# Kernel optimization log

Measured on AMD Instinct MI355X. Metric: run time of the kernel, lower is better.

The kernel has to match this reference:

```python
import jax, jax.numpy as jnp
import numpy as np

N_NODES = 100_000
N_EDGES = 3_200_000
VOCAB = 50_000
D = 256
L_GNN = 4
L_LIN = 2
OUT = 10          # label_size=10 -> output_size=10
N_TGT = 8192
EPS = 1e-5


def layer_norm(x, g, b):
    mu = jnp.mean(x, axis=-1, keepdims=True)
    var = jnp.mean((x - mu) ** 2, axis=-1, keepdims=True)
    return (x - mu) * jax.lax.rsqrt(var + EPS) * g + b


def gcn_conv(x, src, dst, W, b, n):
    # PyG GCNConv defaults: add self loops, symmetric D^-1/2 (A+I) D^-1/2 norm
    h = x @ W                                   # [n, D]
    loops = jnp.arange(n, dtype=src.dtype)
    src2 = jnp.concatenate([src, loops])        # [E+n]
    dst2 = jnp.concatenate([dst, loops])
    deg = jax.ops.segment_sum(jnp.ones(src2.shape[0], dtype=h.dtype), dst2, n)
    dinv = jnp.where(deg > 0, jax.lax.rsqrt(deg), 0.0)
    norm = dinv[src2] * dinv[dst2]              # [E+n]
    out = jax.ops.segment_sum(h[src2] * norm[:, None], dst2, n)  # [n, D]
    return out + b


def setup_inputs() -> dict:
    key = jax.random.key(0)
    ks = jax.random.split(key, 16)
    tokens = jax.random.randint(ks[0], (N_NODES,), 0, VOCAB, dtype=jnp.int32)
    edges = jax.random.randint(ks[1], (2, N_EDGES), 0, N_NODES, dtype=jnp.int32)
    target_indices = jax.random.randint(ks[2], (N_TGT,), 0, N_NODES, dtype=jnp.int32)
    s = 0.05
    emb_table = jax.random.normal(ks[3], (VOCAB, D), jnp.float32)
    gnn_W = jax.random.normal(ks[4], (L_GNN, D, D), jnp.float32) * s
    gnn_b = jnp.zeros((L_GNN, D), jnp.float32)
    gnn_gamma = jnp.ones((L_GNN, D), jnp.float32)
    gnn_beta = jnp.zeros((L_GNN, D), jnp.float32)
    lin_W = jax.random.normal(ks[5], (L_LIN, D, D), jnp.float32) * s
    lin_b = jnp.zeros((L_LIN, D), jnp.float32)
    lin_gamma = jnp.ones((L_LIN, D), jnp.float32)
    lin_beta = jnp.zeros((L_LIN, D), jnp.float32)
    out_W = jax.random.normal(ks[6], (D, OUT), jnp.float32) * s
    out_b = jnp.zeros((OUT,), jnp.float32)
    return {"tokens": tokens, "edges": edges, "target_indices": target_indices,
            "emb_table": emb_table, "gnn_W": gnn_W, "gnn_b": gnn_b,
            "gnn_gamma": gnn_gamma, "gnn_beta": gnn_beta,
            "lin_W": lin_W, "lin_b": lin_b, "lin_gamma": lin_gamma,
            "lin_beta": lin_beta, "out_W": out_W, "out_b": out_b}


def reference(tokens, edges, target_indices, emb_table, gnn_W, gnn_b,
              gnn_gamma, gnn_beta, lin_W, lin_b, lin_gamma, lin_beta,
              out_W, out_b):
    x = emb_table[tokens]                       # [N, D] embedding lookup
    src, dst = edges[0], edges[1]
    for i in range(L_GNN):
        x = gcn_conv(x, src, dst, gnn_W[i], gnn_b[i], N_NODES)
        x = layer_norm(x, gnn_gamma[i], gnn_beta[i])
        x = jax.nn.relu(x)
    x = x[target_indices]                       # [N_TGT, D]
    for i in range(L_LIN):
        x = x @ lin_W[i] + lin_b[i]
        x = layer_norm(x, lin_gamma[i], lin_beta[i])
        x = jax.nn.relu(x)
    return x @ out_W + out_b                    # [N_TGT, OUT]
```

## Files before the change

### kernel.cpp

```cpp
#include <hip/hip_runtime.h>
#include <hip/hip_fp16.h>

#define NN 100000
#define NE 3200000
#define DD 256
#define NT 8192
#define NOUT 10
#define NBUCK 196
#define CSRP_CAP (NE + NBUCK * 4112 + 64)

typedef unsigned short u16;
typedef unsigned int u32;
typedef unsigned char u8;
typedef __attribute__((ext_vector_type(8))) short bf16x8;
typedef __attribute__((ext_vector_type(4))) float f32x4;
typedef __attribute__((ext_vector_type(4))) unsigned int uint4v;

__device__ __forceinline__ float bf2f(u16 u) {
    union { unsigned int i; float f; } v; v.i = ((unsigned int)u) << 16; return v.f;
}
__device__ __forceinline__ u16 f2bf(float f) {
    union { float f; unsigned int i; } v; v.f = f;
    unsigned int x = v.i;
    return (u16)((x + 0x7fffu + ((x >> 16) & 1u)) >> 16);
}
__device__ __forceinline__ unsigned int pack2(float a, float b) {
    return (unsigned int)f2bf(a) | ((unsigned int)f2bf(b) << 16);
}
__device__ __forceinline__ u32 packrec(int src, float w) {
    unsigned short h = __half_as_ushort(__float2half(w));
    return ((u32)src << 15) | (u32)(h & 0x7fff);
}
__device__ __forceinline__ float recw(u32 r) {
    return __half2float(__ushort_as_half((unsigned short)(r & 0x7fff)));
}

__device__ __forceinline__ void gl2lds16(const void* g, void* l) {
    __builtin_amdgcn_global_load_lds(
        (const __attribute__((address_space(1))) unsigned int*)g,
        (__attribute__((address_space(3))) unsigned int*)l, 16, 0, 0);
}

__global__ __launch_bounds__(256) void k_wt(const float* __restrict__ gW,
                                            const float* __restrict__ lW,
                                            u16* __restrict__ Wt,
                                            int* __restrict__ bucketCnt) {
    if (blockIdx.x == 0 && threadIdx.x < NBUCK) bucketCnt[threadIdx.x] = 0;
    int idx = blockIdx.x * 256 + threadIdx.x;
    int l = idx >> 16;
    int nk = idx & 65535;
    int n = nk >> 8, k = nk & 255;
    float v = (l < 4) ? gW[l * 65536 + k * 256 + n]
                      : lW[(l - 4) * 65536 + k * 256 + n];
    Wt[idx] = f2bf(v);
}

__global__ __launch_bounds__(256) void k_binA(const int* __restrict__ dst,
                                              int* __restrict__ bucketCnt) {
    __shared__ int hist[NBUCK];
    int t = threadIdx.x;
    if (t < NBUCK) hist[t] = 0;
    __syncthreads();
    int base = blockIdx.x * 4096;
#pragma unroll
    for (int i = 0; i < 16; i++) {
        int e = base + i * 256 + t;
        if (e < NE) atomicAdd(&hist[dst[e] >> 9], 1);
    }
    __syncthreads();
    if (t < NBUCK && hist[t] > 0) atomicAdd(&bucketCnt[t], hist[t]);
}

__global__ __launch_bounds__(256) void k_bscan(const int* __restrict__ bucketCnt,
                                               int* __restrict__ bucketOff,
                                               int* __restrict__ bucketCur) {
    __shared__ int s[256];
    int t = threadIdx.x;
    int v = (t < NBUCK) ? bucketCnt[t] : 0;
    s[t] = v;
    __syncthreads();
    for (int o = 1; o < 256; o <<= 1) {
        int a = (t >= o) ? s[t - o] : 0;
        __syncthreads();
        s[t] += a;
        __syncthreads();
    }
    if (t < NBUCK) {
        int ex = s[t] - v;
        bucketOff[t] = ex;
        bucketCur[t] = ex;
    }
    if (t == 0) bucketOff[NBUCK] = NE;
}

__global__ __launch_bounds__(1024) void k_binB(const int* __restrict__ src,
                                               const int* __restrict__ dst,
                                               int* __restrict__ bucketCur,
                                               int* __restrict__ recs) {
    __shared__ int hist[NBUCK];
    __shared__ int gbase[NBUCK];
    int t = threadIdx.x;
    if (t < NBUCK) hist[t] = 0;
    __syncthreads();
    int base = blockIdx.x * 16384;
    int recv[16], bks[16], rnk[16];
#pragma unroll
    for (int i = 0; i < 16; i++) {
        int e = base + i * 1024 + t;
        int bk = -1, rec = 0;
        if (e < NE) {
            int s_ = src[e], d_ = dst[e];
            bk = d_ >> 9;
            rec = (s_ << 9) | (d_ & 511);
        }
        bks[i] = bk; recv[i] = rec;
    }
#pragma unroll
    for (int i = 0; i < 16; i++)
        rnk[i] = (bks[i] >= 0) ? atomicAdd(&hist[bks[i]], 1) : 0;
    __syncthreads();
    if (t < NBUCK) {
        int c = hist[t];
        gbase[t] = (c > 0) ? atomicAdd(&bucketCur[t], c) : 0;
    }
    __syncthreads();
#pragma unroll
    for (int i = 0; i < 16; i++)
        if (bks[i] >= 0) {
            int pos = gbase[bks[i]] + rnk[i];
            pos = min(max(pos, 0), NE - 1);
            recs[pos] = recv[i];
        }
}

__global__ __launch_bounds__(256) void k_csrA(const int* __restrict__ recs,
                                              const int* __restrict__ bucketOff,
                                              int2* __restrict__ nodeInfo,
                                              float* __restrict__ dinv,
                                              u32* __restrict__ csrp) {
    __shared__ int cnt[512], off[512];
    int b = blockIdx.x, t = threadIdx.x;
    int beg = min(max(bucketOff[b], 0), NE);
    int end = min(max(bucketOff[b + 1], beg), NE);
    int n = end - beg;
    cnt[t] = 0; cnt[t + 256] = 0;
    __syncthreads();
    for (int i = t; i < n; i += 256)
        atomicAdd(&cnt[recs[beg + i] & 511], 1);
    __syncthreads();
    off[t] = (cnt[t] + 8) & ~7;
    off[t + 256] = (cnt[t + 256] + 8) & ~7;
    __syncthreads();
    for (int o = 1; o < 512; o <<= 1) {
        int v0 = (t >= o) ? off[t - o] : 0;
        int v1 = (t + 256 >= o) ? off[t + 256 - o] : 0;
        __syncthreads();
        off[t] += v0; off[t + 256] += v1;
        __syncthreads();
    }
    int base = (beg + b * 4112 + 7) & ~7;
    for (int k = t; k < 512; k += 256) {
        int node = b * 512 + k;
        if (node >= NN) continue;
        int pd = (cnt[k] + 8) & ~7;
        int nbeg = base + off[k] - pd;
        int2 ni; ni.x = nbeg; ni.y = pd;
        nodeInfo[node] = ni;
        float di = rsqrtf((float)(cnt[k] + 1));
        dinv[node] = di;
        csrp[nbeg] = packrec(node, di * di);
        for (int j = nbeg + 1 + cnt[k]; j < nbeg + pd; j++) csrp[j] = 0u;
    }
}

__global__ __launch_bounds__(256) void k_csrB(const int* __restrict__ recs,
                                              const int* __restrict__ bucketOff,
                                              const int2* __restrict__ nodeInfo,
                                              const float* __restrict__ dinv,
                                              u32* __restrict__ csrp) {
    __shared__ int cur[512];
    int b = blockIdx.x, t = threadIdx.x;
    cur[t] = 0; cur[t + 256] = 0;
    __syncthreads();
    int beg = min(max(bucketOff[b], 0), NE);
    int end = min(max(bucketOff[b + 1], beg), NE);
    int n = end - beg;
    for (int i = t; i < n; i += 256) {
        int r = recs[beg + i];
        int dlow = r & 511;
        int s = min(max(r >> 9, 0), NN - 1);
        int node = b * 512 + dlow;
        int rk = atomicAdd(&cur[dlow], 1);
        int2 ni = nodeInfo[node];
        float w = dinv[s] * dinv[node];
        int pos = ni.x + 1 + rk;
        pos = min(max(pos, 0), CSRP_CAP - 1);
        csrp[pos] = packrec(s, w);
    }
}

#define GEMM_EPILOGUE                                                         \
    for (int i = 0; i < 4; i++)                                               \
        for (int j = 0; j < 4; j++) {                                         \
            int col = colBase + wn * 64 + j * 16 + l16;                       \
            for (int r = 0; r < 4; r++) {                                     \
                int row = rowBase + wm * 64 + i * 16 + quad * 4 + r;          \
                if (row < M) C[row * 256 + col] = f2bf(acc[i][j][r]);         \
            }                                                                 \
        }

#define GEMM_COMPUTE(ASRC, BSRC)                                              \
    for (int ks = 0; ks < 2; ks++) {                                          \
        bf16x8 a_frag[4], b_frag[4];                                          \
        for (int i = 0; i < 4; i++) {                                         \
            int r = wm * 64 + i * 16 + l16;                                   \
            int ch = (ks * 4 + quad) ^ (r & 7);                               \
            a_frag[i] = *(const bf16x8*)(&ASRC[r * 64 + ch * 8]);             \
        }                                                                     \
        for (int j = 0; j < 4; j++) {                                         \
            int r = wn * 64 + j * 16 + l16;                                   \
            int ch = (ks * 4 + quad) ^ (r & 7);                               \
            b_frag[j] = *(const bf16x8*)(&BSRC[r * 64 + ch * 8]);             \
        }                                                                     \
        for (int i = 0; i < 4; i++)                                           \
            for (int j = 0; j < 4; j++)                                       \
                acc[i][j] = __builtin_amdgcn_mfma_f32_16x16x32_bf16(          \
                    a_frag[i], b_frag[j], acc[i][j], 0, 0, 0);                \
    }

#define QUANT_EPILOGUE(Q8, QS)                                                \
    {                                                                         \
        u8* bb = (u8*)As;                          \
        const int gq = blockIdx.y * 2 + wn;                                   \
        float* qsp = QS + (size_t)gq * NN;                                    \
        for (int i = 0; i < 4; i++) {                                         \
            float m0 = 0.f, m1 = 0.f, m2 = 0.f, m3 = 0.f;                     \
            for (int j = 0; j < 4; j++) {                                     \
                m0 = fmaxf(m0, fabsf(acc[i][j][0]));                          \
                m1 = fmaxf(m1, fabsf(acc[i][j][1]));                          \
                m2 = fmaxf(m2, fabsf(acc[i][j][2]));                          \
                m3 = fmaxf(m3, fabsf(acc[i][j][3]));                          \
            }                                                                 \
            for (int o = 1; o < 16; o <<= 1) {                                \
                m0 = fmaxf(m0, __shfl_xor(m0, o, 64));                        \
                m1 = fmaxf(m1, __shfl_xor(m1, o, 64));                        \
                m2 = fmaxf(m2, __shfl_xor(m2, o, 64));                        \
                m3 = fmaxf(m3, __shfl_xor(m3, o, 64));                        \
            }                                                                 \
            float i0 = m0 > 0.f ? 126.f / m0 : 0.f;                           \
            float i1 = m1 > 0.f ? 126.f / m1 : 0.f;                           \
            float i2 = m2 > 0.f ? 126.f / m2 : 0.f;                           \
            float i3 = m3 > 0.f ? 126.f / m3 : 0.f;                           \
            int row0 = rowBase + wm * 64 + i * 16 + quad * 4;                 \
            if (l16 == 0) {                                                   \
                if (row0 + 0 < M) qsp[row0 + 0] = m0 * (1.f / 126.f);         \
                if (row0 + 1 < M) qsp[row0 + 1] = m1 * (1.f / 126.f);         \
                if (row0 + 2 < M) qsp[row0 + 2] = m2 * (1.f / 126.f);         \
                if (row0 + 3 < M) qsp[row0 + 3] = m3 * (1.f / 126.f);         \
            }                                                                 \
            int rb = (wm * 64 + i * 16 + quad * 4) * 128;                     \
            for (int j = 0; j < 4; j++) {                                     \
                int cb = wn * 64 + j * 16 + l16;                              \
                bb[rb + cb]       = (u8)((int)rintf(acc[i][j][0]*i0) + 128);  \
                bb[rb + 128 + cb] = (u8)((int)rintf(acc[i][j][1]*i1) + 128);  \
                bb[rb + 256 + cb] = (u8)((int)rintf(acc[i][j][2]*i2) + 128);  \
                bb[rb + 384 + cb] = (u8)((int)rintf(acc[i][j][3]*i3) + 128);  \
            }                                                                 \
        }                                                                     \
        __syncthreads();                                                      \
        for (int u = tid; u < 1024; u += 256) {                               \
            int r = u >> 3, c16 = (u & 7) * 16;                               \
            int row = rowBase + r;                                            \
            if (row < M)                                                      \
                *(uint4*)(Q8 + (size_t)row * 256 + colBase + c16) =           \
                    *(const uint4*)(bb + r * 128 + c16);                      \
        }                                                                     \
    }

__global__ __launch_bounds__(256) void k_gemm(const u16* __restrict__ A,
                                              const u16* __restrict__ Bt,
                                              u16* __restrict__ C, int M) {
    __shared__ __align__(16) u16 As[128 * 64];
    __shared__ __align__(16) u16 Bs[128 * 64];
    const int tid = threadIdx.x;
    const int wave = tid >> 6, lane = tid & 63;
    const int wm = wave >> 1, wn = wave & 1;
    const int rowBase = blockIdx.x * 128;
    const int colBase = blockIdx.y * 128;
    const int quad = lane >> 4, l16 = lane & 15;

    f32x4 acc[4][4] = {};

    for (int kk = 0; kk < 4; kk++) {
        int k0 = kk * 64;
#pragma unroll
        for (int i = 0; i < 4; i++) {
            int j = (i * 4 + wave) * 64 + lane;
            int r = j >> 3, c = j & 7;
            int cg = c ^ (r & 7);
            int ga = rowBase + r; if (ga >= M) ga = M - 1;
            gl2lds16(A + (size_t)ga * 256 + k0 + cg * 8,
                     &As[(i * 4 + wave) * 512]);
            gl2lds16(Bt + (size_t)(colBase + r) * 256 + k0 + cg * 8,
                     &Bs[(i * 4 + wave) * 512]);
        }
        __syncthreads();
        GEMM_COMPUTE(As, Bs)
        __syncthreads();
    }
    GEMM_EPILOGUE
}

__global__ __launch_bounds__(256) void k_gemmq(const u16* __restrict__ A,
                                               const u16* __restrict__ Bt,
                                               u8* __restrict__ q8,
                                               float* __restrict__ qs, int M) {
    __shared__ __align__(16) u16 As[128 * 64];
    __shared__ __align__(16) u16 Bs[128 * 64];
    const int tid = threadIdx.x;
    const int wave = tid >> 6, lane = tid & 63;
    const int wm = wave >> 1, wn = wave & 1;
    const int rowBase = blockIdx.x * 128;
    const int colBase = blockIdx.y * 128;
    const int quad = lane >> 4, l16 = lane & 15;

    f32x4 acc[4][4] = {};

    for (int kk = 0; kk < 4; kk++) {
        int k0 = kk * 64;
#pragma unroll
        for (int i = 0; i < 4; i++) {
            int j = (i * 4 + wave) * 64 + lane;
            int r = j >> 3, c = j & 7;
            int cg = c ^ (r & 7);
            int ga = rowBase + r; if (ga >= M) ga = M - 1;
            gl2lds16(A + (size_t)ga * 256 + k0 + cg * 8,
                     &As[(i * 4 + wave) * 512]);
            gl2lds16(Bt + (size_t)(colBase + r) * 256 + k0 + cg * 8,
                     &Bs[(i * 4 + wave) * 512]);
        }
        __syncthreads();
        GEMM_COMPUTE(As, Bs)
        __syncthreads();
    }
    QUANT_EPILOGUE(q8, qs)
}

__global__ __launch_bounds__(256) void k_gemm_embq(const int* __restrict__ tokens,
                                                   const float* __restrict__ emb,
                                                   const u16* __restrict__ Bt,
                                                   u8* __restrict__ q8,
                                                   float* __restrict__ qs, int M) {
    __shared__ __align__(16) u16 As[128 * 64];
    __shared__ __align__(16) u16 Bs[128 * 64];
    __shared__ int tokLDS[128];
    const int tid = threadIdx.x;
    const int wave = tid >> 6, lane = tid & 63;
    const int wm = wave >> 1, wn = wave & 1;
    const int rowBase = blockIdx.x * 128;
    const int colBase = blockIdx.y * 128;
    const int quad = lane >> 4, l16 = lane & 15;

    if (tid < 128) {
        int ga = rowBase + tid; if (ga >= M) ga = M - 1;
        tokLDS[tid] = tokens[ga];
    }
    f32x4 acc[4][4] = {};
    __syncthreads();

    for (int kk = 0; kk < 4; kk++) {
        int k0 = kk * 64;
#pragma unroll
        for (int i = 0; i < 4; i++) {
            int j = (i * 4 + wave) * 64 + lane;
            int r = j >> 3, c = j & 7;
            int cg = c ^ (r & 7);
            const float* srcp = emb + (size_t)tokLDS[r] * 256 + k0 + cg * 8;
            float4 f0 = *(const float4*)srcp;
            float4 f1 = *(const float4*)(srcp + 4);
            uint4 pk;
            pk.x = pack2(f0.x, f0.y); pk.y = pack2(f0.z, f0.w);
            pk.z = pack2(f1.x, f1.y); pk.w = pack2(f1.z, f1.w);
            *(uint4*)(&As[j * 8]) = pk;
            gl2lds16(Bt + (size_t)(colBase + r) * 256 + k0 + cg * 8,
                     &Bs[(i * 4 + wave) * 512]);
        }
        __syncthreads();
        GEMM_COMPUTE(As, Bs)
        __syncthreads();
    }
    QUANT_EPILOGUE(q8, qs)
}

__global__ __launch_bounds__(256) void k_gemm_gather(const u16* __restrict__ X,
                                                     const int* __restrict__ tgt,
                                                     const u16* __restrict__ Bt,
                                                     u16* __restrict__ C, int M) {
    __shared__ __align__(16) u16 As[128 * 64];
    __shared__ __align__(16) u16 Bs[128 * 64];
    __shared__ int rowLDS[128];
    const int tid = threadIdx.x;
    const int wave = tid >> 6, lane = tid & 63;
    const int wm = wave >> 1, wn = wave & 1;
    const int rowBase = blockIdx.x * 128;
    const int colBase = blockIdx.y * 128;
    const int quad = lane >> 4, l16 = lane & 15;

    if (tid < 128) {
        int ga = rowBase + tid; if (ga >= M) ga = M - 1;
        rowLDS[tid] = tgt[ga];
    }
    f32x4 acc[4][4] = {};
    __syncthreads();

    for (int kk = 0; kk < 4; kk++) {
        int k0 = kk * 64;
#pragma unroll
        for (int i = 0; i < 4; i++) {
            int j = (i * 4 + wave) * 64 + lane;
            int r = j >> 3, c = j & 7;
            int cg = c ^ (r & 7);
            uint4 v = *(const uint4*)(X + (size_t)rowLDS[r] * 256 + k0 + cg * 8);
            *(uint4*)(&As[j * 8]) = v;
            gl2lds16(Bt + (size_t)(colBase + r) * 256 + k0 + cg * 8,
                     &Bs[(i * 4 + wave) * 512]);
        }
        __syncthreads();
        GEMM_COMPUTE(As, Bs)
        __syncthreads();
    }
    GEMM_EPILOGUE
}

#define GF8(RR, Q0, Q1, Q2, Q3, W0, W1, W2, W3)                               \
    {                                                                         \
        int s0 = (int)(RR.x >> 15), s1 = (int)(RR.y >> 15);                   \
        int s2 = (int)(RR.z >> 15), s3 = (int)(RR.w >> 15);                   \
        Q0 = *(const uint2*)(qb + (size_t)s0 * 256);                          \
        Q1 = *(const uint2*)(qb + (size_t)s1 * 256);                          \
        Q2 = *(const uint2*)(qb + (size_t)s2 * 256);                          \
        Q3 = *(const uint2*)(qb + (size_t)s3 * 256);                          \
        W0 = recw(RR.x) * qsp[s0]; W1 = recw(RR.y) * qsp[s1];                 \
        W2 = recw(RR.z) * qsp[s2]; W3 = recw(RR.w) * qsp[s3];                 \
    }

#define GC8_ONE(Q, W)                                                         \
    {                                                                         \
        Ks += W;                                                              \
        a0 = fmaf(W, (float)(Q.x & 255u), a0);                                \
        a1 = fmaf(W, (float)((Q.x >> 8) & 255u), a1);                         \
        a2 = fmaf(W, (float)((Q.x >> 16) & 255u), a2);                        \
        a3 = fmaf(W, (float)(Q.x >> 24), a3);                                 \
        a4 = fmaf(W, (float)(Q.y & 255u), a4);                                \
        a5 = fmaf(W, (float)((Q.y >> 8) & 255u), a5);                         \
        a6 = fmaf(W, (float)((Q.y >> 16) & 255u), a6);                        \
        a7 = fmaf(W, (float)(Q.y >> 24), a7);                                 \
    }

__global__ __launch_bounds__(256) void k_aggr(const u8* __restrict__ q8,
                                              const float* __restrict__ qs,
                                              const int2* __restrict__ nodeInfo,
                                              const u32* __restrict__ csrp,
                                              const float* __restrict__ bias,
                                              const float* __restrict__ gamma,
                                              const float* __restrict__ beta,
                                              u16* __restrict__ xo) {
    const int wave = threadIdx.x >> 6, lane = threadIdx.x & 63;
    const int half = lane >> 5, l32 = lane & 31;
    const int node = blockIdx.x * 4 + wave;
    const int d8 = l32 * 8;
    int2 ni = nodeInfo[node];
    float a0=0,a1=0,a2=0,a3=0,a4=0,a5=0,a6=0,a7=0;
    float Ks = 0.0f;
    const u8* qb = q8 + d8;
    const float* qsp = qs + (size_t)(l32 >> 3) * NN;
    const u32* cp = csrp + ni.x + half * 4;
    const int nrec = ni.y;
    int j = 0;
    for (; j + 16 <= nrec; j += 16, cp += 16) {
        uint4v ra = __builtin_nontemporal_load((const uint4v*)cp);
        uint4v rb = __builtin_nontemporal_load((const uint4v*)(cp + 8));
        uint2 qa0, qa1, qa2, qa3, qb0, qb1, qb2, qb3;
        float wa0, wa1, wa2, wa3, wb0, wb1, wb2, wb3;
        GF8(ra, qa0, qa1, qa2, qa3, wa0, wa1, wa2, wa3);
        GF8(rb, qb0, qb1, qb2, qb3, wb0, wb1, wb2, wb3);
        GC8_ONE(qa0, wa0); GC8_ONE(qa1, wa1);
        GC8_ONE(qa2, wa2); GC8_ONE(qa3, wa3);
        GC8_ONE(qb0, wb0); GC8_ONE(qb1, wb1);
        GC8_ONE(qb2, wb2); GC8_ONE(qb3, wb3);
    }
    if (j < nrec) {
        uint4v ra = __builtin_nontemporal_load((const uint4v*)cp);
        uint2 qa0, qa1, qa2, qa3;
        float wa0, wa1, wa2, wa3;
        GF8(ra, qa0, qa1, qa2, qa3, wa0, wa1, wa2, wa3);
        GC8_ONE(qa0, wa0); GC8_ONE(qa1, wa1);
        GC8_ONE(qa2, wa2); GC8_ONE(qa3, wa3);
    }
    a0 += __shfl_xor(a0, 32, 64); a1 += __shfl_xor(a1, 32, 64);
    a2 += __shfl_xor(a2, 32, 64); a3 += __shfl_xor(a3, 32, 64);
    a4 += __shfl_xor(a4, 32, 64); a5 += __shfl_xor(a5, 32, 64);
    a6 += __shfl_xor(a6, 32, 64); a7 += __shfl_xor(a7, 32, 64);
    Ks += __shfl_xor(Ks, 32, 64);
    float c128 = 128.0f * Ks;
    a0 -= c128; a1 -= c128; a2 -= c128; a3 -= c128;
    a4 -= c128; a5 -= c128; a6 -= c128; a7 -= c128;

    float4 b0 = *(const float4*)(bias + d8);
    float4 b1 = *(const float4*)(bias + d8 + 4);
    a0 += b0.x; a1 += b0.y; a2 += b0.z; a3 += b0.w;
    a4 += b1.x; a5 += b1.y; a6 += b1.z; a7 += b1.w;
    float s1 = a0+a1+a2+a3+a4+a5+a6+a7;
    float s2 = a0*a0+a1*a1+a2*a2+a3*a3+a4*a4+a5*a5+a6*a6+a7*a7;
    for (int o = 16; o >= 1; o >>= 1) {
        s1 += __shfl_xor(s1, o, 64);
        s2 += __shfl_xor(s2, o, 64);
    }
    float mean = s1 * (1.0f / 256.0f);
    float var = s2 * (1.0f / 256.0f) - mean * mean;
    float rstd = rsqrtf(var + 1e-5f);
    if (half == 0) {
        float4 g0 = *(const float4*)(gamma + d8);
        float4 g1 = *(const float4*)(gamma + d8 + 4);
        float4 e0 = *(const float4*)(beta + d8);
        float4 e1 = *(const float4*)(beta + d8 + 4);
        float y0 = fmaxf((a0 - mean) * rstd * g0.x + e0.x, 0.0f);
        float y1 = fmaxf((a1 - mean) * rstd * g0.y + e0.y, 0.0f);
        float y2 = fmaxf((a2 - mean) * rstd * g0.z + e0.z, 0.0f);
        float y3 = fmaxf((a3 - mean) * rstd * g0.w + e0.w, 0.0f);
        float y4 = fmaxf((a4 - mean) * rstd * g1.x + e1.x, 0.0f);
        float y5 = fmaxf((a5 - mean) * rstd * g1.y + e1.y, 0.0f);
        float y6 = fmaxf((a6 - mean) * rstd * g1.z + e1.z, 0.0f);
        float y7 = fmaxf((a7 - mean) * rstd * g1.w + e1.w, 0.0f);
        uint4v o;
        o.x = pack2(y0, y1);
        o.y = pack2(y2, y3);
        o.z = pack2(y4, y5);
        o.w = pack2(y6, y7);
        __builtin_nontemporal_store(o, (uint4v*)(xo + node * 256 + d8));
    }
}

__global__ __launch_bounds__(256) void k_lnrelu(const u16* __restrict__ h,
                                                const float* __restrict__ bias,
                                                const float* __restrict__ gamma,
                                                const float* __restrict__ beta,
                                                u16* __restrict__ xo) {
    int wave = threadIdx.x >> 6, lane = threadIdx.x & 63;
    int row = blockIdx.x * 4 + wave;
    int base = row * 256 + lane * 4;
    ushort4 hv = *(const ushort4*)(h + base);
    float4 bv = *(const float4*)(bias + lane * 4);
    float a0 = bf2f(hv.x) + bv.x, a1 = bf2f(hv.y) + bv.y;
    float a2 = bf2f(hv.z) + bv.z, a3 = bf2f(hv.w) + bv.w;
    float s1 = a0 + a1 + a2 + a3;
    float s2 = a0 * a0 + a1 * a1 + a2 * a2 + a3 * a3;
    for (int o = 32; o >= 1; o >>= 1) {
        s1 += __shfl_xor(s1, o, 64);
        s2 += __shfl_xor(s2, o, 64);
    }
    float mean = s1 * (1.0f / 256.0f);
    float var = s2 * (1.0f / 256.0f) - mean * mean;
    float rstd = rsqrtf(var + 1e-5f);
    float4 gv = *(const float4*)(gamma + lane * 4);
    float4 be = *(const float4*)(beta + lane * 4);
    float y0 = fmaxf((a0 - mean) * rstd * gv.x + be.x, 0.0f);
    float y1 = fmaxf((a1 - mean) * rstd * gv.y + be.y, 0.0f);
    float y2 = fmaxf((a2 - mean) * rstd * gv.z + be.z, 0.0f);
    float y3 = fmaxf((a3 - mean) * rstd * gv.w + be.w, 0.0f);
    ushort4 o4;
    o4.x = f2bf(y0); o4.y = f2bf(y1); o4.z = f2bf(y2); o4.w = f2bf(y3);
    *(ushort4*)(xo + base) = o4;
}

__global__ __launch_bounds__(256) void k_lnout(const u16* __restrict__ h,
                                               const float* __restrict__ bias,
                                               const float* __restrict__ gamma,
                                               const float* __restrict__ beta,
                                               const float* __restrict__ W,
                                               const float* __restrict__ ob,
                                               float* __restrict__ out) {
    __shared__ float Ws[DD * NOUT];
    int tid = threadIdx.x;
    for (int i = tid; i < DD * NOUT; i += 256) Ws[i] = W[i];
    __syncthreads();
    int wave = tid >> 6, lane = tid & 63;
    int row = blockIdx.x * 4 + wave;
    int base = row * 256 + lane * 4;
    ushort4 hv = *(const ushort4*)(h + base);
    float4 bv = *(const float4*)(bias + lane * 4);
    float a0 = bf2f(hv.x) + bv.x, a1 = bf2f(hv.y) + bv.y;
    float a2 = bf2f(hv.z) + bv.z, a3 = bf2f(hv.w) + bv.w;
    float s1 = a0 + a1 + a2 + a3;
    float s2 = a0 * a0 + a1 * a1 + a2 * a2 + a3 * a3;
    for (int o = 32; o >= 1; o >>= 1) {
        s1 += __shfl_xor(s1, o, 64);
        s2 += __shfl_xor(s2, o, 64);
    }
    float mean = s1 * (1.0f / 256.0f);
    float var = s2 * (1.0f / 256.0f) - mean * mean;
    float rstd = rsqrtf(var + 1e-5f);
    float4 gv = *(const float4*)(gamma + lane * 4);
    float4 be = *(const float4*)(beta + lane * 4);
    float y0 = bf2f(f2bf(fmaxf((a0 - mean) * rstd * gv.x + be.x, 0.0f)));
    float y1 = bf2f(f2bf(fmaxf((a1 - mean) * rstd * gv.y + be.y, 0.0f)));
    float y2 = bf2f(f2bf(fmaxf((a2 - mean) * rstd * gv.z + be.z, 0.0f)));
    float y3 = bf2f(f2bf(fmaxf((a3 - mean) * rstd * gv.w + be.w, 0.0f)));
    int d = lane * 4;
    for (int o = 0; o < NOUT; o++) {
        float p = y0 * Ws[(d + 0) * NOUT + o] + y1 * Ws[(d + 1) * NOUT + o] +
                  y2 * Ws[(d + 2) * NOUT + o] + y3 * Ws[(d + 3) * NOUT + o];
        for (int off = 32; off >= 1; off >>= 1) p += __shfl_xor(p, off, 64);
        if (lane == 0) out[row * NOUT + o] = p + ob[o];
    }
}

extern "C" void kernel_launch(void* const* d_in, const int* in_sizes, int n_in,
                              void* d_out, int out_size, void* d_ws, size_t ws_size,
                              hipStream_t stream) {
    (void)in_sizes; (void)n_in; (void)out_size; (void)ws_size;
    const int* tokens = (const int*)d_in[0];
    const int* edges = (const int*)d_in[1];
    const int* tgt = (const int*)d_in[2];
    const float* emb = (const float*)d_in[3];
    const float* gnn_W = (const float*)d_in[4];
    const float* gnn_b = (const float*)d_in[5];
    const float* gnn_g = (const float*)d_in[6];
    const float* gnn_be = (const float*)d_in[7];
    const float* lin_W = (const float*)d_in[8];
    const float* lin_b = (const float*)d_in[9];
    const float* lin_g = (const float*)d_in[10];
    const float* lin_be = (const float*)d_in[11];
    const float* out_W = (const float*)d_in[12];
    const float* out_b = (const float*)d_in[13];
    float* out = (float*)d_out;

    char* ws = (char*)d_ws;
    u16* x = (u16*)ws;           ws += (size_t)NN * 256 * 2;
    char* hreg = ws;             ws += (size_t)NN * 256 * 2;
    int* recs = (int*)hreg;
    u32* csrp = (u32*)ws;        ws += (size_t)CSRP_CAP * 4;
    int2* nodeInfo = (int2*)ws;  ws += (size_t)NN * 8;
    float* dinv = (float*)ws;    ws += (size_t)NN * 4;
    int* bucketCnt = (int*)ws;   ws += 256 * 4;
    int* bucketOff = (int*)ws;   ws += 256 * 4;
    int* bucketCur = (int*)ws;   ws += 256 * 4;
    u16* Wt = (u16*)ws;          ws += (size_t)6 * 65536 * 2;
    u16* xt = (u16*)ws;          ws += (size_t)NT * 256 * 2;
    u16* ht = (u16*)ws;          ws += (size_t)NT * 256 * 2;
    u8* q8 = (u8*)ws;            ws += (size_t)NN * 256;
    float* qs = (float*)ws;      ws += (size_t)4 * NN * 4;

    const int* e_src = edges;
    const int* e_dst = edges + NE;

    k_wt<<<1536, 256, 0, stream>>>(gnn_W, lin_W, Wt, bucketCnt);
    k_binA<<<782, 256, 0, stream>>>(e_dst, bucketCnt);
    k_bscan<<<1, 256, 0, stream>>>(bucketCnt, bucketOff, bucketCur);
    k_binB<<<196, 1024, 0, stream>>>(e_src, e_dst, bucketCur, recs);
    k_csrA<<<NBUCK, 256, 0, stream>>>(recs, bucketOff, nodeInfo, dinv, csrp);
    k_csrB<<<NBUCK, 256, 0, stream>>>(recs, bucketOff, nodeInfo, dinv, csrp);

    for (int l = 0; l < 4; l++) {
        if (l == 0)
            k_gemm_embq<<<dim3(782, 2), 256, 0, stream>>>(tokens, emb, Wt,
                                                          q8, qs, NN);
        else
            k_gemmq<<<dim3(782, 2), 256, 0, stream>>>(x, Wt + l * 65536,
                                                      q8, qs, NN);
        k_aggr<<<25000, 256, 0, stream>>>(q8, qs, nodeInfo, csrp,
                                          gnn_b + l * 256, gnn_g + l * 256,
                                          gnn_be + l * 256, x);
    }
    k_gemm_gather<<<dim3(64, 2), 256, 0, stream>>>(x, tgt, Wt + 4 * 65536,
                                                   ht, NT);
    k_lnrelu<<<2048, 256, 0, stream>>>(ht, lin_b, lin_g, lin_be, xt);
    k_gemm<<<dim3(64, 2), 256, 0, stream>>>(xt, Wt + 5 * 65536, ht, NT);
    k_lnout<<<2048, 256, 0, stream>>>(ht, lin_b + 256, lin_g + 256,
                                      lin_be + 256, out_W, out_b, out);
}
```

Baseline: 1.087 ms.

## Quantize full 256-wide rows with one scale per row in GEMM tiles

```diff
diff --git a/kernel.cpp b/kernel.cpp
--- a/kernel.cpp
+++ b/kernel.cpp
@@ -228,52 +228,65 @@
                     a_frag[i], b_frag[j], acc[i][j], 0, 0, 0);                \
     }
 
-#define QUANT_EPILOGUE(Q8, QS)                                                \
+#define GEMMQ_COMPUTE                                                         \
+    for (int ks = 0; ks < 2; ks++) {                                          \
+        bf16x8 a_frag[4], b_frag[4];                                          \
+        for (int i = 0; i < 4; i++) {                                         \
+            int r = i * 16 + l16;                                             \
+            int ch = (ks * 4 + quad) ^ (r & 7);                               \
+            a_frag[i] = *(const bf16x8*)(&As[r * 64 + ch * 8]);               \
+        }                                                                     \
+        for (int j = 0; j < 4; j++) {                                         \
+            int r = wn * 64 + j * 16 + l16;                                   \
+            int ch = (ks * 4 + quad) ^ (r & 7);                               \
+            b_frag[j] = *(const bf16x8*)(&Bs[r * 64 + ch * 8]);               \
+        }                                                                     \
+        for (int i = 0; i < 4; i++)                                           \
+            for (int j = 0; j < 4; j++)                                       \
+                acc[i][j] = __builtin_amdgcn_mfma_f32_16x16x32_bf16(          \
+                    a_frag[i], b_frag[j], acc[i][j], 0, 0, 0);                \
+    }
+
+#define QUANTQ_EPILOGUE(Q8, QS)                                               \
     {                                                                         \
-        u8* bb = (u8*)As;                          \
-        const int gq = blockIdx.y * 2 + wn;                                   \
-        float* qsp = QS + (size_t)gq * NN;                                    \
-        for (int i = 0; i < 4; i++) {                                         \
-            float m0 = 0.f, m1 = 0.f, m2 = 0.f, m3 = 0.f;                     \
-            for (int j = 0; j < 4; j++) {                                     \
-                m0 = fmaxf(m0, fabsf(acc[i][j][0]));                          \
-                m1 = fmaxf(m1, fabsf(acc[i][j][1]));                          \
-                m2 = fmaxf(m2, fabsf(acc[i][j][2]));                          \
-                m3 = fmaxf(m3, fabsf(acc[i][j][3]));                          \
+        float* rowmaxLDS = (float*)As;                           \
+        for (int i = 0; i < 4; i++)                                           \
+            for (int r = 0; r < 4; r++) {                                     \
+                float m = 0.f;                                                \
+                for (int j = 0; j < 4; j++)                                   \
+                    m = fmaxf(m, fabsf(acc[i][j][r]));                        \
+                m = fmaxf(m, __shfl_xor(m, 1, 64));                           \
+                m = fmaxf(m, __shfl_xor(m, 2, 64));                           \
+                m = fmaxf(m, __shfl_xor(m, 4, 64));                           \
+                m = fmaxf(m, __shfl_xor(m, 8, 64));                           \
+                if (l16 == 0)                                                 \
+                    rowmaxLDS[wn * 64 + i * 16 + quad * 4 + r] = m;           \
             }                                                                 \
-            for (int o = 1; o < 16; o <<= 1) {                                \
-                m0 = fmaxf(m0, __shfl_xor(m0, o, 64));                        \
-                m1 = fmaxf(m1, __shfl_xor(m1, o, 64));                        \
-                m2 = fmaxf(m2, __shfl_xor(m2, o, 64));                        \
-                m3 = fmaxf(m3, __shfl_xor(m3, o, 64));                        \
+        __syncthreads();                                                      \
+        u8* bb = (u8*)Bs;                                      \
+        for (int i = 0; i < 4; i++)                                           \
+            for (int r = 0; r < 4; r++) {                                     \
+                int rl = i * 16 + quad * 4 + r;                               \
+                float m = fmaxf(fmaxf(rowmaxLDS[rl], rowmaxLDS[64 + rl]),     \
+                                fmaxf(rowmaxLDS[128 + rl],                    \
+                                      rowmaxLDS[192 + rl]));                  \
+                if (wn == 0 && l16 == 0) {                                    \
+                    int row = rowBase + rl;                                   \
+                    if (row < M) QS[row] = m * (1.0f / 126.0f);               \
+                }                                                             \
+                float inv = m > 0.f ? 126.f / m : 0.f;                        \
+                for (int j = 0; j < 4; j++)                                   \
+                    bb[rl * 256 + wn * 64 + j * 16 + l16] =                   \
+                        (u8)((int)rintf(acc[i][j][r] * inv) + 128);           \
             }                                                                 \
-            float i0 = m0 > 0.f ? 126.f / m0 : 0.f;                           \
-            float i1 = m1 > 0.f ? 126.f / m1 : 0.f;                           \
-            float i2 = m2 > 0.f ? 126.f / m2 : 0.f;                           \
-            float i3 = m3 > 0.f ? 126.f / m3 : 0.f;                           \
-            int row0 = rowBase + wm * 64 + i * 16 + quad * 4;                 \
-            if (l16 == 0) {                                                   \
-                if (row0 + 0 < M) qsp[row0 + 0] = m0 * (1.f / 126.f);         \
-                if (row0 + 1 < M) qsp[row0 + 1] = m1 * (1.f / 126.f);         \
-                if (row0 + 2 < M) qsp[row0 + 2] = m2 * (1.f / 126.f);         \
-                if (row0 + 3 < M) qsp[row0 + 3] = m3 * (1.f / 126.f);         \
-            }                                                                 \
-            int rb = (wm * 64 + i * 16 + quad * 4) * 128;                     \
-            for (int j = 0; j < 4; j++) {                                     \
-                int cb = wn * 64 + j * 16 + l16;                              \
-                bb[rb + cb]       = (u8)((int)rintf(acc[i][j][0]*i0) + 128);  \
-                bb[rb + 128 + cb] = (u8)((int)rintf(acc[i][j][1]*i1) + 128);  \
-                bb[rb + 256 + cb] = (u8)((int)rintf(acc[i][j][2]*i2) + 128);  \
-                bb[rb + 384 + cb] = (u8)((int)rintf(acc[i][j][3]*i3) + 128);  \
-            }                                                                 \
-        }                                                                     \
         __syncthreads();                                                      \
-        for (int u = tid; u < 1024; u += 256) {                               \
-            int r = u >> 3, c16 = (u & 7) * 16;                               \
-            int row = rowBase + r;                                            \
+        for (int u = 0; u < 4; u++) {                                         \
+            int v = u * 256 + tid;                                            \
+            int rl = v >> 4, c16 = (v & 15) * 16;                             \
+            int row = rowBase + rl;                                           \
             if (row < M)                                                      \
-                *(uint4*)(Q8 + (size_t)row * 256 + colBase + c16) =           \
-                    *(const uint4*)(bb + r * 128 + c16);                      \
+                *(uint4*)(Q8 + (size_t)row * 256 + c16) =                     \
+                    *(const uint4*)(bb + rl * 256 + c16);                     \
         }                                                                     \
     }
 
@@ -315,13 +328,12 @@
                                                const u16* __restrict__ Bt,
                                                u8* __restrict__ q8,
                                                float* __restrict__ qs, int M) {
-    __shared__ __align__(16) u16 As[128 * 64];
-    __shared__ __align__(16) u16 Bs[128 * 64];
+    __shared__ __align__(16) u16 As[64 * 64];
+    __shared__ __align__(16) u16 Bs[256 * 64];
     const int tid = threadIdx.x;
     const int wave = tid >> 6, lane = tid & 63;
-    const int wm = wave >> 1, wn = wave & 1;
-    const int rowBase = blockIdx.x * 128;
-    const int colBase = blockIdx.y * 128;
+    const int wn = wave;
+    const int rowBase = blockIdx.x * 64;
     const int quad = lane >> 4, l16 = lane & 15;
 
     f32x4 acc[4][4] = {};
@@ -329,21 +341,27 @@
     for (int kk = 0; kk < 4; kk++) {
         int k0 = kk * 64;
 #pragma unroll
-        for (int i = 0; i < 4; i++) {
+        for (int i = 0; i < 2; i++) {
             int j = (i * 4 + wave) * 64 + lane;
             int r = j >> 3, c = j & 7;
             int cg = c ^ (r & 7);
             int ga = rowBase + r; if (ga >= M) ga = M - 1;
             gl2lds16(A + (size_t)ga * 256 + k0 + cg * 8,
                      &As[(i * 4 + wave) * 512]);
-            gl2lds16(Bt + (size_t)(colBase + r) * 256 + k0 + cg * 8,
+        }
+#pragma unroll
+        for (int i = 0; i < 8; i++) {
+            int j = (i * 4 + wave) * 64 + lane;
+            int r = j >> 3, c = j & 7;
+            int cg = c ^ (r & 7);
+            gl2lds16(Bt + (size_t)r * 256 + k0 + cg * 8,
                      &Bs[(i * 4 + wave) * 512]);
         }
         __syncthreads();
-        GEMM_COMPUTE(As, Bs)
-        __syncthreads();
-    }
-    QUANT_EPILOGUE(q8, qs)
+        GEMMQ_COMPUTE
+        __syncthreads();
+    }
+    QUANTQ_EPILOGUE(q8, qs)
 }
 
 __global__ __launch_bounds__(256) void k_gemm_embq(const int* __restrict__ tokens,
@@ -351,17 +369,16 @@
                                                    const u16* __restrict__ Bt,
                                                    u8* __restrict__ q8,
                                                    float* __restrict__ qs, int M) {
-    __shared__ __align__(16) u16 As[128 * 64];
-    __shared__ __align__(16) u16 Bs[128 * 64];
-    __shared__ int tokLDS[128];
+    __shared__ __align__(16) u16 As[64 * 64];
+    __shared__ __align__(16) u16 Bs[256 * 64];
+    __shared__ int tokLDS[64];
     const int tid = threadIdx.x;
     const int wave = tid >> 6, lane = tid & 63;
-    const int wm = wave >> 1, wn = wave & 1;
-    const int rowBase = blockIdx.x * 128;
-    const int colBase = blockIdx.y * 128;
+    const int wn = wave;
+    const int rowBase = blockIdx.x * 64;
     const int quad = lane >> 4, l16 = lane & 15;
 
-    if (tid < 128) {
+    if (tid < 64) {
         int ga = rowBase + tid; if (ga >= M) ga = M - 1;
         tokLDS[tid] = tokens[ga];
     }
@@ -371,7 +388,7 @@
     for (int kk = 0; kk < 4; kk++) {
         int k0 = kk * 64;
 #pragma unroll
-        for (int i = 0; i < 4; i++) {
+        for (int i = 0; i < 2; i++) {
             int j = (i * 4 + wave) * 64 + lane;
             int r = j >> 3, c = j & 7;
             int cg = c ^ (r & 7);
@@ -382,14 +399,20 @@
             pk.x = pack2(f0.x, f0.y); pk.y = pack2(f0.z, f0.w);
             pk.z = pack2(f1.x, f1.y); pk.w = pack2(f1.z, f1.w);
             *(uint4*)(&As[j * 8]) = pk;
-            gl2lds16(Bt + (size_t)(colBase + r) * 256 + k0 + cg * 8,
+        }
+#pragma unroll
+        for (int i = 0; i < 8; i++) {
+            int j = (i * 4 + wave) * 64 + lane;
+            int r = j >> 3, c = j & 7;
+            int cg = c ^ (r & 7);
+            gl2lds16(Bt + (size_t)r * 256 + k0 + cg * 8,
                      &Bs[(i * 4 + wave) * 512]);
         }
         __syncthreads();
-        GEMM_COMPUTE(As, Bs)
-        __syncthreads();
-    }
-    QUANT_EPILOGUE(q8, qs)
+        GEMMQ_COMPUTE
+        __syncthreads();
+    }
+    QUANTQ_EPILOGUE(q8, qs)
 }
 
 __global__ __launch_bounds__(256) void k_gemm_gather(const u16* __restrict__ X,
@@ -440,8 +463,8 @@
         Q1 = *(const uint2*)(qb + (size_t)s1 * 256);                          \
         Q2 = *(const uint2*)(qb + (size_t)s2 * 256);                          \
         Q3 = *(const uint2*)(qb + (size_t)s3 * 256);                          \
-        W0 = recw(RR.x) * qsp[s0]; W1 = recw(RR.y) * qsp[s1];                 \
-        W2 = recw(RR.z) * qsp[s2]; W3 = recw(RR.w) * qsp[s3];                 \
+        W0 = recw(RR.x) * qs[s0]; W1 = recw(RR.y) * qs[s1];                   \
+        W2 = recw(RR.z) * qs[s2]; W3 = recw(RR.w) * qs[s3];                   \
     }
 
 #define GC8_ONE(Q, W)                                                         \
@@ -473,7 +496,6 @@
     float a0=0,a1=0,a2=0,a3=0,a4=0,a5=0,a6=0,a7=0;
     float Ks = 0.0f;
     const u8* qb = q8 + d8;
-    const float* qsp = qs + (size_t)(l32 >> 3) * NN;
     const u32* cp = csrp + ni.x + half * 4;
     const int nrec = ni.y;
     int j = 0;
@@ -648,8 +670,8 @@
     u16* Wt = (u16*)ws;          ws += (size_t)6 * 65536 * 2;
     u16* xt = (u16*)ws;          ws += (size_t)NT * 256 * 2;
     u16* ht = (u16*)ws;          ws += (size_t)NT * 256 * 2;
-    u8* q8 = (u8*)ws;            ws += (size_t)NN * 256;
-    float* qs = (float*)ws;      ws += (size_t)4 * NN * 4;
+    u8* q8 = (u8*)ws;            ws += (size_t)(NN + 64) * 256;
+    float* qs = (float*)ws;      ws += (size_t)(NN + 64) * 4;
 
     const int* e_src = edges;
     const int* e_dst = edges + NE;
@@ -663,11 +685,11 @@
 
     for (int l = 0; l < 4; l++) {
         if (l == 0)
-            k_gemm_embq<<<dim3(782, 2), 256, 0, stream>>>(tokens, emb, Wt,
-                                                          q8, qs, NN);
+            k_gemm_embq<<<1563, 256, 0, stream>>>(tokens, emb, Wt,
+                                                  q8, qs, NN);
         else
-            k_gemmq<<<dim3(782, 2), 256, 0, stream>>>(x, Wt + l * 65536,
-                                                      q8, qs, NN);
+            k_gemmq<<<1563, 256, 0, stream>>>(x, Wt + l * 65536,
+                                              q8, qs, NN);
         k_aggr<<<25000, 256, 0, stream>>>(q8, qs, nodeInfo, csrp,
                                           gnn_b + l * 256, gnn_g + l * 256,
                                           gnn_be + l * 256, x);
```

Result: faster. 954.2 us, median of 2 (-12.2%).

## Restructure quantizing GEMM to full-width row tiles with register-resident weights

Applied to the files above, without the earlier changes.

```diff
diff --git a/kernel.cpp b/kernel.cpp
--- a/kernel.cpp
+++ b/kernel.cpp
@@ -228,11 +228,43 @@
                     a_frag[i], b_frag[j], acc[i][j], 0, 0, 0);                \
     }
 
-#define QUANT_EPILOGUE(Q8, QS)                                                \
+__global__ __launch_bounds__(256) void k_gemm(const u16* __restrict__ A,
+                                              const u16* __restrict__ Bt,
+                                              u16* __restrict__ C, int M) {
+    __shared__ __align__(16) u16 As[128 * 64];
+    __shared__ __align__(16) u16 Bs[128 * 64];
+    const int tid = threadIdx.x;
+    const int wave = tid >> 6, lane = tid & 63;
+    const int wm = wave >> 1, wn = wave & 1;
+    const int rowBase = blockIdx.x * 128;
+    const int colBase = blockIdx.y * 128;
+    const int quad = lane >> 4, l16 = lane & 15;
+
+    f32x4 acc[4][4] = {};
+
+    for (int kk = 0; kk < 4; kk++) {
+        int k0 = kk * 64;
+#pragma unroll
+        for (int i = 0; i < 4; i++) {
+            int j = (i * 4 + wave) * 64 + lane;
+            int r = j >> 3, c = j & 7;
+            int cg = c ^ (r & 7);
+            int ga = rowBase + r; if (ga >= M) ga = M - 1;
+            gl2lds16(A + (size_t)ga * 256 + k0 + cg * 8,
+                     &As[(i * 4 + wave) * 512]);
+            gl2lds16(Bt + (size_t)(colBase + r) * 256 + k0 + cg * 8,
+                     &Bs[(i * 4 + wave) * 512]);
+        }
+        __syncthreads();
+        GEMM_COMPUTE(As, Bs)
+        __syncthreads();
+    }
+    GEMM_EPILOGUE
+}
+
+#define GQ_EPILOGUE(Q8, QS)                                                   \
     {                                                                         \
-        u8* bb = (u8*)As;                          \
-        const int gq = blockIdx.y * 2 + wn;                                   \
-        float* qsp = QS + (size_t)gq * NN;                                    \
+                                \
         for (int i = 0; i < 4; i++) {                                         \
             float m0 = 0.f, m1 = 0.f, m2 = 0.f, m3 = 0.f;                     \
             for (int j = 0; j < 4; j++) {                                     \
@@ -247,149 +279,128 @@
                 m2 = fmaxf(m2, __shfl_xor(m2, o, 64));                        \
                 m3 = fmaxf(m3, __shfl_xor(m3, o, 64));                        \
             }                                                                 \
-            float i0 = m0 > 0.f ? 126.f / m0 : 0.f;                           \
-            float i1 = m1 > 0.f ? 126.f / m1 : 0.f;                           \
-            float i2 = m2 > 0.f ? 126.f / m2 : 0.f;                           \
-            float i3 = m3 > 0.f ? 126.f / m3 : 0.f;                           \
-            int row0 = rowBase + wm * 64 + i * 16 + quad * 4;                 \
             if (l16 == 0) {                                                   \
-                if (row0 + 0 < M) qsp[row0 + 0] = m0 * (1.f / 126.f);         \
-                if (row0 + 1 < M) qsp[row0 + 1] = m1 * (1.f / 126.f);         \
-                if (row0 + 2 < M) qsp[row0 + 2] = m2 * (1.f / 126.f);         \
-                if (row0 + 3 < M) qsp[row0 + 3] = m3 * (1.f / 126.f);         \
-            }                                                                 \
-            int rb = (wm * 64 + i * 16 + quad * 4) * 128;                     \
-            for (int j = 0; j < 4; j++) {                                     \
-                int cb = wn * 64 + j * 16 + l16;                              \
-                bb[rb + cb]       = (u8)((int)rintf(acc[i][j][0]*i0) + 128);  \
-                bb[rb + 128 + cb] = (u8)((int)rintf(acc[i][j][1]*i1) + 128);  \
-                bb[rb + 256 + cb] = (u8)((int)rintf(acc[i][j][2]*i2) + 128);  \
-                bb[rb + 384 + cb] = (u8)((int)rintf(acc[i][j][3]*i3) + 128);  \
+                int rl = wr * 64 + i * 16 + quad * 4;                         \
+                rmax[wc][rl + 0] = m0; rmax[wc][rl + 1] = m1;                 \
+                rmax[wc][rl + 2] = m2; rmax[wc][rl + 3] = m3;                 \
             }                                                                 \
         }                                                                     \
         __syncthreads();                                                      \
-        for (int u = tid; u < 1024; u += 256) {                               \
-            int r = u >> 3, c16 = (u & 7) * 16;                               \
-            int row = rowBase + r;                                            \
-            if (row < M)                                                      \
-                *(uint4*)(Q8 + (size_t)row * 256 + colBase + c16) =           \
-                    *(const uint4*)(bb + r * 128 + c16);                      \
+        for (int i = 0; i < 4; i++) {                                         \
+            int rl = wr * 64 + i * 16 + quad * 4;                             \
+            for (int r = 0; r < 4; r++) {                                     \
+                float m = fmaxf(fmaxf(rmax[0][rl + r], rmax[1][rl + r]),      \
+                                fmaxf(rmax[2][rl + r], rmax[3][rl + r]));     \
+                if (wc == 0 && l16 == 0) {                                    \
+                    int row = rowBase + rl + r;                               \
+                    if (row < M) QS[row] = m * (1.0f / 126.0f);               \
+                }                                                             \
+                float inv = m > 0.f ? 126.f / m : 0.f;                        \
+                for (int j = 0; j < 4; j++)                                   \
+                    sc[(rl + r) * 256 + wc * 64 + j * 16 + l16] =             \
+                        (u8)((int)rintf(acc[i][j][r] * inv) + 128);           \
+            }                                                                 \
         }                                                                     \
-    }
-
-__global__ __launch_bounds__(256) void k_gemm(const u16* __restrict__ A,
-                                              const u16* __restrict__ Bt,
-                                              u16* __restrict__ C, int M) {
-    __shared__ __align__(16) u16 As[128 * 64];
-    __shared__ __align__(16) u16 Bs[128 * 64];
+        __syncthreads();                                                      \
+        for (int it = 0; it < 4; it++) {                                      \
+            int id = it * 512 + tid;                                          \
+            int row = id >> 4, c16 = (id & 15) * 16;                          \
+            int grow = rowBase + row;                                         \
+            if (grow < M)                                                     \
+                *(uint4*)(Q8 + (size_t)grow * 256 + c16) =                    \
+                    *(const uint4*)(sc + row * 256 + c16);                    \
+        }                                                                     \
+    }
+
+#define GQ_LOAD_B                                                             \
+    bf16x8 breg[4][8];                                                        \
+    _Pragma("unroll")                                                         \
+    for (int j = 0; j < 4; j++) {                                             \
+        int col = wc * 64 + j * 16 + l16;                                     \
+        _Pragma("unroll")                                                     \
+        for (int ks = 0; ks < 8; ks++)                                        \
+            breg[j][ks] =                                                     \
+                *(const bf16x8*)(Bt + (size_t)col * 256 + ks * 32 + quad * 8);\
+    }
+
+__global__ __launch_bounds__(512, 2) void k_gemmq(const u16* __restrict__ A,
+                                                  const u16* __restrict__ Bt,
+                                                  u8* __restrict__ q8,
+                                                  float* __restrict__ qs, int M) {
+    __shared__ __align__(16) u8 sc[128 * 256];
+    __shared__ float rmax[4][128];
     const int tid = threadIdx.x;
     const int wave = tid >> 6, lane = tid & 63;
-    const int wm = wave >> 1, wn = wave & 1;
+    const int wr = wave >> 2, wc = wave & 3;
+    const int quad = lane >> 4, l16 = lane & 15;
     const int rowBase = blockIdx.x * 128;
-    const int colBase = blockIdx.y * 128;
-    const int quad = lane >> 4, l16 = lane & 15;
-
+
+    GQ_LOAD_B
+    int arow[4];
+#pragma unroll
+    for (int i = 0; i < 4; i++) {
+        int r = rowBase + wr * 64 + i * 16 + l16;
+        arow[i] = (r < M) ? r : (M - 1);
+    }
     f32x4 acc[4][4] = {};
-
-    for (int kk = 0; kk < 4; kk++) {
-        int k0 = kk * 64;
-#pragma unroll
-        for (int i = 0; i < 4; i++) {
-            int j = (i * 4 + wave) * 64 + lane;
-            int r = j >> 3, c = j & 7;
-            int cg = c ^ (r & 7);
-            int ga = rowBase + r; if (ga >= M) ga = M - 1;
-            gl2lds16(A + (size_t)ga * 256 + k0 + cg * 8,
-                     &As[(i * 4 + wave) * 512]);
-            gl2lds16(Bt + (size_t)(colBase + r) * 256 + k0 + cg * 8,
-                     &Bs[(i * 4 + wave) * 512]);
-        }
-        __syncthreads();
-        GEMM_COMPUTE(As, Bs)
-        __syncthreads();
-    }
-    GEMM_EPILOGUE
-}
-
-__global__ __launch_bounds__(256) void k_gemmq(const u16* __restrict__ A,
-                                               const u16* __restrict__ Bt,
-                                               u8* __restrict__ q8,
-                                               float* __restrict__ qs, int M) {
-    __shared__ __align__(16) u16 As[128 * 64];
-    __shared__ __align__(16) u16 Bs[128 * 64];
+#pragma unroll
+    for (int ks = 0; ks < 8; ks++) {
+        bf16x8 af[4];
+#pragma unroll
+        for (int i = 0; i < 4; i++)
+            af[i] = *(const bf16x8*)(A + (size_t)arow[i] * 256 + ks * 32 +
+                                     quad * 8);
+#pragma unroll
+        for (int i = 0; i < 4; i++)
+#pragma unroll
+            for (int j = 0; j < 4; j++)
+                acc[i][j] = __builtin_amdgcn_mfma_f32_16x16x32_bf16(
+                    af[i], breg[j][ks], acc[i][j], 0, 0, 0);
+    }
+    GQ_EPILOGUE(q8, qs)
+}
+
+__global__ __launch_bounds__(512, 2) void k_gemm_embq(
+        const int* __restrict__ tokens, const float* __restrict__ emb,
+        const u16* __restrict__ Bt, u8* __restrict__ q8,
+        float* __restrict__ qs, int M) {
+    __shared__ __align__(16) u8 sc[128 * 256];
+    __shared__ float rmax[4][128];
     const int tid = threadIdx.x;
     const int wave = tid >> 6, lane = tid & 63;
-    const int wm = wave >> 1, wn = wave & 1;
+    const int wr = wave >> 2, wc = wave & 3;
+    const int quad = lane >> 4, l16 = lane & 15;
     const int rowBase = blockIdx.x * 128;
-    const int colBase = blockIdx.y * 128;
-    const int quad = lane >> 4, l16 = lane & 15;
-
+
+    GQ_LOAD_B
+    int tok[4];
+#pragma unroll
+    for (int i = 0; i < 4; i++) {
+        int r = rowBase + wr * 64 + i * 16 + l16;
+        tok[i] = tokens[(r < M) ? r : (M - 1)];
+    }
     f32x4 acc[4][4] = {};
-
-    for (int kk = 0; kk < 4; kk++) {
-        int k0 = kk * 64;
+#pragma unroll
+    for (int ks = 0; ks < 8; ks++) {
+        bf16x8 af[4];
 #pragma unroll
         for (int i = 0; i < 4; i++) {
-            int j = (i * 4 + wave) * 64 + lane;
-            int r = j >> 3, c = j & 7;
-            int cg = c ^ (r & 7);
-            int ga = rowBase + r; if (ga >= M) ga = M - 1;
-            gl2lds16(A + (size_t)ga * 256 + k0 + cg * 8,
-                     &As[(i * 4 + wave) * 512]);
-            gl2lds16(Bt + (size_t)(colBase + r) * 256 + k0 + cg * 8,
-                     &Bs[(i * 4 + wave) * 512]);
-        }
-        __syncthreads();
-        GEMM_COMPUTE(As, Bs)
-        __syncthreads();
-    }
-    QUANT_EPILOGUE(q8, qs)
-}
-
-__global__ __launch_bounds__(256) void k_gemm_embq(const int* __restrict__ tokens,
-                                                   const float* __restrict__ emb,
-                                                   const u16* __restrict__ Bt,
-                                                   u8* __restrict__ q8,
-                                                   float* __restrict__ qs, int M) {
-    __shared__ __align__(16) u16 As[128 * 64];
-    __shared__ __align__(16) u16 Bs[128 * 64];
-    __shared__ int tokLDS[128];
-    const int tid = threadIdx.x;
-    const int wave = tid >> 6, lane = tid & 63;
-    const int wm = wave >> 1, wn = wave & 1;
-    const int rowBase = blockIdx.x * 128;
-    const int colBase = blockIdx.y * 128;
-    const int quad = lane >> 4, l16 = lane & 15;
-
-    if (tid < 128) {
-        int ga = rowBase + tid; if (ga >= M) ga = M - 1;
-        tokLDS[tid] = tokens[ga];
-    }
-    f32x4 acc[4][4] = {};
-    __syncthreads();
-
-    for (int kk = 0; kk < 4; kk++) {
-        int k0 = kk * 64;
-#pragma unroll
-        for (int i = 0; i < 4; i++) {
-            int j = (i * 4 + wave) * 64 + lane;
-            int r = j >> 3, c = j & 7;
-            int cg = c ^ (r & 7);
-            const float* srcp = emb + (size_t)tokLDS[r] * 256 + k0 + cg * 8;
-            float4 f0 = *(const float4*)srcp;
-            float4 f1 = *(const float4*)(srcp + 4);
+            const float* sp = emb + (size_t)tok[i] * 256 + ks * 32 + quad * 8;
+            float4 f0 = *(const float4*)sp;
+            float4 f1 = *(const float4*)(sp + 4);
             uint4 pk;
             pk.x = pack2(f0.x, f0.y); pk.y = pack2(f0.z, f0.w);
             pk.z = pack2(f1.x, f1.y); pk.w = pack2(f1.z, f1.w);
-            *(uint4*)(&As[j * 8]) = pk;
-            gl2lds16(Bt + (size_t)(colBase + r) * 256 + k0 + cg * 8,
-                     &Bs[(i * 4 + wave) * 512]);
+            af[i] = *(bf16x8*)&pk;
         }
-        __syncthreads();
-        GEMM_COMPUTE(As, Bs)
-        __syncthreads();
-    }
-    QUANT_EPILOGUE(q8, qs)
+#pragma unroll
+        for (int i = 0; i < 4; i++)
+#pragma unroll
+            for (int j = 0; j < 4; j++)
+                acc[i][j] = __builtin_amdgcn_mfma_f32_16x16x32_bf16(
+                    af[i], breg[j][ks], acc[i][j], 0, 0, 0);
+    }
+    GQ_EPILOGUE(q8, qs)
 }
 
 __global__ __launch_bounds__(256) void k_gemm_gather(const u16* __restrict__ X,
@@ -440,8 +451,8 @@
         Q1 = *(const uint2*)(qb + (size_t)s1 * 256);                          \
         Q2 = *(const uint2*)(qb + (size_t)s2 * 256);                          \
         Q3 = *(const uint2*)(qb + (size_t)s3 * 256);                          \
-        W0 = recw(RR.x) * qsp[s0]; W1 = recw(RR.y) * qsp[s1];                 \
-        W2 = recw(RR.z) * qsp[s2]; W3 = recw(RR.w) * qsp[s3];                 \
+        W0 = recw(RR.x) * qs[s0]; W1 = recw(RR.y) * qs[s1];                   \
+        W2 = recw(RR.z) * qs[s2]; W3 = recw(RR.w) * qs[s3];                   \
     }
 
 #define GC8_ONE(Q, W)                                                         \
@@ -473,7 +484,6 @@
     float a0=0,a1=0,a2=0,a3=0,a4=0,a5=0,a6=0,a7=0;
     float Ks = 0.0f;
     const u8* qb = q8 + d8;
-    const float* qsp = qs + (size_t)(l32 >> 3) * NN;
     const u32* cp = csrp + ni.x + half * 4;
     const int nrec = ni.y;
     int j = 0;
@@ -648,8 +658,8 @@
     u16* Wt = (u16*)ws;          ws += (size_t)6 * 65536 * 2;
     u16* xt = (u16*)ws;          ws += (size_t)NT * 256 * 2;
     u16* ht = (u16*)ws;          ws += (size_t)NT * 256 * 2;
-    u8* q8 = (u8*)ws;            ws += (size_t)NN * 256;
-    float* qs = (float*)ws;      ws += (size_t)4 * NN * 4;
+    u8* q8 = (u8*)ws;            ws += (size_t)(NN + 128) * 256;
+    float* qs = (float*)ws;      ws += (size_t)(NN + 128) * 4;
 
     const int* e_src = edges;
     const int* e_dst = edges + NE;
@@ -663,11 +673,11 @@
 
     for (int l = 0; l < 4; l++) {
         if (l == 0)
-            k_gemm_embq<<<dim3(782, 2), 256, 0, stream>>>(tokens, emb, Wt,
-                                                          q8, qs, NN);
+            k_gemm_embq<<<782, 512, 0, stream>>>(tokens, emb, Wt,
+                                                 q8, qs, NN);
         else
-            k_gemmq<<<dim3(782, 2), 256, 0, stream>>>(x, Wt + l * 65536,
-                                                      q8, qs, NN);
+            k_gemmq<<<782, 512, 0, stream>>>(x, Wt + l * 65536,
+                                             q8, qs, NN);
         k_aggr<<<25000, 256, 0, stream>>>(q8, qs, nodeInfo, csrp,
                                           gnn_b + l * 256, gnn_g + l * 256,
                                           gnn_be + l * 256, x);
```

After: 1.135 ms. +4.4%, slower.
